# Performance work log

Measured on AMD Instinct MI355X. Metric: run time of the kernel, lower is better.

The kernel has to match this reference:

```python
import jax, jax.numpy as jnp
import numpy as np

B, T, D, H = 2, 2048, 1024, 16
DK = D // H
NEG = -1e9  # stand-in for -inf; causal mask guarantees >=1 valid key per row


def setup_inputs() -> dict:
    key = jax.random.key(0)
    ks = jax.random.split(key, 9)
    s = 1.0 / np.sqrt(D)
    x = jax.random.normal(ks[0], (B, T, D), dtype=jnp.float32)
    mask = jnp.broadcast_to(jnp.tril(jnp.ones((T, T), dtype=jnp.int32))[None, None], (B, 1, T, T))
    params = {}
    for i, n in enumerate(['q', 'k', 'v', 'o']):
        params['W' + n] = jax.random.normal(ks[1 + 2 * i], (D, D), dtype=jnp.float32) * s
        params['b' + n] = jax.random.normal(ks[2 + 2 * i], (D,), dtype=jnp.float32) * s
    return dict(x=x, mask=mask, **params)


def reference(x, mask, Wq, bq, Wk, bk, Wv, bv, Wo, bo):
    Bx, Tx, Dx = x.shape
    # projections: [B,T,D] -> [B,H,T,DK]
    def split_heads(y):
        return y.reshape(Bx, Tx, H, DK).transpose(0, 2, 1, 3)
    Q = split_heads(x @ Wq + bq)
    K = split_heads(x @ Wk + bk)
    V = split_heads(x @ Wv + bv)
    scores = jnp.einsum('bhqd,bhkd->bhqk', Q, K) / jnp.sqrt(jnp.float32(DK))
    scores = jnp.where(mask == 0, NEG, scores)
    attn = jax.nn.softmax(scores, axis=-1)  # dropout is identity in eval / p=0
    out = jnp.einsum('bhqk,bhkd->bhqd', attn, V)
    out = out.transpose(0, 2, 1, 3).reshape(Bx, Tx, Dx)
    return out @ Wo + bo
```

## Files before the change

kernel.cpp:

```cpp
#include <hip/hip_runtime.h>
#include <hip/hip_bf16.h>

typedef __bf16 bf16;
typedef __attribute__((ext_vector_type(8))) __bf16 bf16x8;
typedef __attribute__((ext_vector_type(4))) __bf16 bf16x4;
typedef __attribute__((ext_vector_type(4))) float f32x4;

#define TSEQ 2048
#define DMODEL 1024
#define NHEAD 16
#define DKH 64
#define BATCH 2
#define NQKV 3072

typedef __attribute__((address_space(1))) const void gv_t;
typedef __attribute__((address_space(3))) void sv_t;
__device__ __forceinline__ void gll16(const bf16* g, bf16* s) {
    __builtin_amdgcn_global_load_lds((gv_t*)g, (sv_t*)s, 16, 0, 0);
}
__device__ __forceinline__ void wait_vm0() {
    __builtin_amdgcn_s_waitcnt(0x0F70);
}

#define PREP_CONV 4096
#define PREP_TW   4096
#define PREP_GRID (PREP_CONV + PREP_TW + 12)
__global__ __launch_bounds__(256) void prep(
    const float* __restrict__ x,
    const float* __restrict__ Wq, const float* __restrict__ Wk,
    const float* __restrict__ Wv, const float* __restrict__ Wo,
    const float* __restrict__ bq, const float* __restrict__ bk,
    const float* __restrict__ bv,
    bf16* __restrict__ xb, bf16* __restrict__ WT, float* __restrict__ biasO)
{
    __shared__ float t[32][33];
    int bid = blockIdx.x;
    const int tid = threadIdx.x;
    if (bid < PREP_CONV) {
        int i = (bid * 256 + tid) * 4;
        f32x4 v = *(const f32x4*)(x + i);
        bf16x4 o;
#pragma unroll
        for (int j = 0; j < 4; ++j) o[j] = (bf16)v[j];
        *(bf16x4*)(xb + i) = o;
        return;
    }
    bid -= PREP_CONV;
    if (bid < PREP_TW) {
        int z = bid >> 10;
        int by = ((bid >> 5) & 31) * 32, bx = (bid & 31) * 32;
        const float* W = z == 0 ? Wq : z == 1 ? Wk : z == 2 ? Wv : Wo;
        bf16* T = WT + (size_t)z * DMODEL * DMODEL;
        int tx = tid & 31, ty = tid >> 5;
#pragma unroll
        for (int i = 0; i < 4; ++i)
            t[ty + i * 8][tx] = W[(size_t)(by + ty + i * 8) * DMODEL + bx + tx];
        __syncthreads();
#pragma unroll
        for (int i = 0; i < 4; ++i)
            T[(size_t)(bx + ty + i * 8) * DMODEL + by + tx] = (bf16)t[tx][ty + i * 8];
        return;
    }
    bid -= PREP_TW;
    int i = bid * 256 + tid;
    float v = i < 1024 ? bq[i] : i < 2048 ? bk[i - 1024] : bv[i - 2048];
    biasO[i] = v;
}

__global__ __launch_bounds__(256) void transpose_v(
    const bf16* __restrict__ QKV, bf16* __restrict__ VT)
{
    __shared__ bf16 t[32][33];
    int b = blockIdx.z >> 4, h = blockIdx.z & 15;
    int t0 = blockIdx.x * 32, d0 = blockIdx.y * 32;
    int tx = threadIdx.x, ty = threadIdx.y;
#pragma unroll
    for (int i = 0; i < 4; ++i)
        t[ty + i * 8][tx] =
            QKV[(size_t)(b * TSEQ + t0 + ty + i * 8) * NQKV + 2048 + h * DKH + d0 + tx];
    __syncthreads();
#pragma unroll
    for (int i = 0; i < 4; ++i)
        VT[((size_t)(b * NHEAD + h) * DKH + d0 + ty + i * 8) * TSEQ + t0 + tx] =
            t[tx][ty + i * 8];
}

template <typename OutT, int NW_N>
__global__ __launch_bounds__(256) void gemm_bias_kernel(
    const bf16* __restrict__ A, const bf16* __restrict__ BT,
    const float* __restrict__ bias, OutT* __restrict__ C, int ldc)
{
    constexpr int BN    = NW_N * 64;
    constexpr int MW    = 4 / NW_N;
    constexpr int WROWS = 128 / MW;
    constexpr int FM    = WROWS / 16;
    constexpr int ASZ   = 128 * 32;
    constexpr int BSZ   = BN * 32;
    constexpr int BNP   = BN + 4;
    constexpr int EPI   = sizeof(OutT) == 2 ? 128 * BN : 64 * BNP * 2;
    constexpr int SMEM  = (2 * ASZ + 2 * BSZ) > EPI ? (2 * ASZ + 2 * BSZ) : EPI;
    __shared__ bf16 smem[SMEM];
    bf16* As0 = smem;
    bf16* Bs0 = smem + 2 * ASZ;

    const int tid = threadIdx.x;
    const int ln = tid & 63, wave = tid >> 6;
    const int wm = NW_N == 2 ? (wave >> 1) : wave;
    const int wn = NW_N == 2 ? (wave & 1) : 0;
    const int lr = ln & 15, quad = ln >> 4;
    const int m0 = blockIdx.y * 128, n0 = blockIdx.x * BN;

    f32x4 acc[FM][4] = {};

    const int grow = ln >> 2;
    const int gcol = (ln & 3) * 8;
    const bf16* Ag = A + (size_t)(m0 + wave * 32 + grow) * DMODEL + gcol;
    const bf16* Bg = BT + (size_t)(n0 + (NW_N == 2 ? wave * 32 : wave * 16) + grow) * DMODEL + gcol;

    auto stage = [&](int buf, int kk) {
        bf16* AsW = As0 + buf * ASZ + wave * 1024;
        gll16(Ag + kk, AsW);
        gll16(Ag + (size_t)16 * DMODEL + kk, AsW + 512);
        if constexpr (NW_N == 2) {
            bf16* BsW = Bs0 + buf * BSZ + wave * 1024;
            gll16(Bg + kk, BsW);
            gll16(Bg + (size_t)16 * DMODEL + kk, BsW + 512);
        } else {
            gll16(Bg + kk, Bs0 + buf * BSZ + wave * 512);
        }
    };

    constexpr int NT = DMODEL / 32;
    stage(0, 0);
    wait_vm0();
    __syncthreads();
    for (int kt = 0; kt < NT; ++kt) {
        if (kt + 1 < NT) stage((kt + 1) & 1, (kt + 1) * 32);
        const bf16* AsB = As0 + (kt & 1) * ASZ;
        const bf16* BsB = Bs0 + (kt & 1) * BSZ;
        bf16x8 af[FM], bfr[4];
#pragma unroll
        for (int i = 0; i < FM; ++i)
            af[i] = *(const bf16x8*)(AsB + (wm * WROWS + i * 16 + lr) * 32 + quad * 8);
#pragma unroll
        for (int j = 0; j < 4; ++j)
            bfr[j] = *(const bf16x8*)(BsB + (wn * 64 + j * 16 + lr) * 32 + quad * 8);
#pragma unroll
        for (int i = 0; i < FM; ++i)
#pragma unroll
            for (int j = 0; j < 4; ++j)
                acc[i][j] = __builtin_amdgcn_mfma_f32_16x16x32_bf16(
                    af[i], bfr[j], acc[i][j], 0, 0, 0);
        wait_vm0();
        __syncthreads();
    }

    if constexpr (sizeof(OutT) == 2) {
        bf16* Cs = smem;
#pragma unroll
        for (int j = 0; j < 4; ++j) {
            int nl = wn * 64 + j * 16 + lr;
            float bv = bias[n0 + nl];
#pragma unroll
            for (int i = 0; i < FM; ++i) {
                int ml = wm * WROWS + i * 16 + quad * 4;
#pragma unroll
                for (int r = 0; r < 4; ++r)
                    Cs[(ml + r) * BN + nl] = (bf16)(acc[i][j][r] + bv);
            }
        }
        __syncthreads();
        constexpr int LPR = BN / 8;
        constexpr int RPP = 256 / LPR;
        const int rr = tid / LPR, cc = (tid % LPR) * 8;
#pragma unroll
        for (int p = 0; p < 128 / RPP; ++p) {
            int row = p * RPP + rr;
            *(bf16x8*)(C + (size_t)(m0 + row) * ldc + n0 + cc) =
                *(const bf16x8*)(Cs + row * BN + cc);
        }
    } else {
        float* Cf = (float*)smem;
#pragma unroll
        for (int half = 0; half < 2; ++half) {
            if (((wm * WROWS) >> 6) == half) {
#pragma unroll
                for (int j = 0; j < 4; ++j) {
                    int nl = wn * 64 + j * 16 + lr;
                    float bv = bias[n0 + nl];
#pragma unroll
                    for (int i = 0; i < FM; ++i) {
                        int ml = wm * WROWS + i * 16 + quad * 4 - half * 64;
#pragma unroll
                        for (int r = 0; r < 4; ++r)
                            Cf[(ml + r) * BNP + nl] = acc[i][j][r] + bv;
                    }
                }
            }
            __syncthreads();
            constexpr int LPR = BN / 4;
            constexpr int RPP = 256 / LPR;
            const int rr = tid / LPR, cc = (tid % LPR) * 4;
#pragma unroll
            for (int p = 0; p < 64 / RPP; ++p) {
                int row = p * RPP + rr;
                *(f32x4*)(C + (size_t)(m0 + half * 64 + row) * ldc + n0 + cc) =
                    *(const f32x4*)(Cf + row * BNP + cc);
            }
            __syncthreads();
        }
    }
}

template <bool MASK>
__device__ __forceinline__ void attn_chunk(
    int kc, int q0w, int lr, int quad,
    const bf16* __restrict__ KsB, const bf16* __restrict__ VsB,
    bf16* __restrict__ Pw,
    const bf16x8 qb[2], f32x4 oacc[4], float& lrow)
{
    const int sw = lr & 7;
    bf16x8 kb[4][2];
#pragma unroll
    for (int kt = 0; kt < 4; ++kt)
#pragma unroll
        for (int kk = 0; kk < 2; ++kk)
            kb[kt][kk] = *(const bf16x8*)(KsB + (kt * 16 + lr) * 64 +
                                          (((kk * 4 + quad) ^ sw) * 8));
    f32x4 st[4] = {};
#pragma unroll
    for (int kt = 0; kt < 4; ++kt)
#pragma unroll
        for (int kk = 0; kk < 2; ++kk)
            st[kt] = __builtin_amdgcn_mfma_f32_16x16x32_bf16(
                kb[kt][kk], qb[kk], st[kt], 0, 0, 0);

    const float scale2 = 0.18033688f;
    const int q = q0w + lr;
    float rs = 0.f;
#pragma unroll
    for (int kt = 0; kt < 4; ++kt) {
        bf16x4 p4;
#pragma unroll
        for (int r = 0; r < 4; ++r) {
            float p = exp2f(fmaf(st[kt][r], scale2, -24.0f));
            if (MASK && (kc + kt * 16 + quad * 4 + r > q)) p = 0.f;
            rs += p;
            p4[r] = (bf16)p;
        }
        *(bf16x4*)(Pw + lr * 64 + (((kt * 2 + (quad >> 1)) ^ sw) * 8) +
                   (quad & 1) * 4) = p4;
    }
    rs += __shfl_xor(rs, 16);
    rs += __shfl_xor(rs, 32);
    lrow += rs;

#pragma unroll
    for (int kk = 0; kk < 2; ++kk) {
        bf16x8 pa = *(const bf16x8*)(Pw + lr * 64 + (((kk * 4 + quad) ^ sw) * 8));
#pragma unroll
        for (int dt = 0; dt < 4; ++dt) {
            bf16x8 vb = *(const bf16x8*)(VsB + (dt * 16 + lr) * 64 +
                                         (((kk * 4 + quad) ^ sw) * 8));
            oacc[dt] = __builtin_amdgcn_mfma_f32_16x16x32_bf16(
                pa, vb, oacc[dt], 0, 0, 0);
        }
    }
}

__global__ __launch_bounds__(256, 4) void flash_attn(
    const bf16* __restrict__ QKV, const bf16* __restrict__ VT,
    bf16* __restrict__ O)
{
    __shared__ bf16 Ks[2][64 * 64];
    __shared__ bf16 Vs[2][64 * 64];
    __shared__ bf16 Pl[4][16 * 64];
    const int tid = threadIdx.x;
    const int ln = tid & 63, w = tid >> 6;
    const int lr = ln & 15, quad = ln >> 4;
    const int h = blockIdx.y, b = blockIdx.z;

    int xb = blockIdx.x;
    if ((h ^ b) & 1) xb = (TSEQ / 64 - 1) - xb;
    const int q0 = xb * 64;
    const int q0w = q0 + w * 16;
    bf16* Pw = Pl[w];

    const bf16* Qb = QKV + (size_t)b * TSEQ * NQKV + h * DKH;
    const bf16* Kb = Qb + 1024;
    const bf16* VTb = VT + (size_t)(b * NHEAD + h) * DKH * TSEQ;

    const int srow = (w & 1) * 32 + (ln >> 3);
    const int scol = ((ln & 7) ^ ((ln >> 3) & 7)) * 8;
    const bool stK = (w < 2);

    auto stage = [&](int buf, int kc) {
        if (stK) {
            const bf16* g = Kb + (size_t)(kc + srow) * NQKV + scol;
            bf16* s = &Ks[buf][(w & 1) * 32 * 64];
#pragma unroll
            for (int l = 0; l < 4; ++l)
                gll16(g + (size_t)(l * 8) * NQKV, s + l * 8 * 64);
        } else {
            const bf16* g = VTb + (size_t)srow * TSEQ + kc + scol;
            bf16* s = &Vs[buf][(w & 1) * 32 * 64];
#pragma unroll
            for (int l = 0; l < 4; ++l)
                gll16(g + (size_t)(l * 8) * TSEQ, s + l * 8 * 64);
        }
    };

    bf16x8 qb[2];
#pragma unroll
    for (int kk = 0; kk < 2; ++kk)
        qb[kk] = *(const bf16x8*)(Qb + (size_t)(q0w + lr) * NQKV +
                                  kk * 32 + quad * 8);

    f32x4 oacc[4] = {};
    float lrow = 0.f;

    const int nch = xb + 1;
    stage(0, 0);
    wait_vm0();
    __syncthreads();
    for (int c = 0; c < nch; ++c) {
        if (c + 1 < nch) stage((c + 1) & 1, (c + 1) * 64);
        const int kc = c * 64;
        if (c + 1 < nch)
            attn_chunk<false>(kc, q0w, lr, quad, Ks[c & 1], Vs[c & 1], Pw,
                              qb, oacc, lrow);
        else
            attn_chunk<true>(kc, q0w, lr, quad, Ks[c & 1], Vs[c & 1], Pw,
                             qb, oacc, lrow);
        wait_vm0();
        __syncthreads();
    }

#pragma unroll
    for (int r = 0; r < 4; ++r) {
        float inv = 1.0f / __shfl(lrow, quad * 4 + r);
        int row = q0w + quad * 4 + r;
#pragma unroll
        for (int dt = 0; dt < 4; ++dt)
            O[(size_t)(b * TSEQ + row) * DMODEL + h * DKH + dt * 16 + lr] =
                (bf16)(oacc[dt][r] * inv);
    }
}

extern "C" void kernel_launch(void* const* d_in, const int* in_sizes, int n_in,
                              void* d_out, int out_size, void* d_ws, size_t ws_size,
                              hipStream_t stream)
{
    const float* x  = (const float*)d_in[0];
    const float* Wq = (const float*)d_in[2];
    const float* bq = (const float*)d_in[3];
    const float* Wk = (const float*)d_in[4];
    const float* bk = (const float*)d_in[5];
    const float* Wv = (const float*)d_in[6];
    const float* bv = (const float*)d_in[7];
    const float* Wo = (const float*)d_in[8];
    const float* bo = (const float*)d_in[9];

    char* ws = (char*)d_ws;
    bf16* xb   = (bf16*)(ws);
    bf16* QKV  = (bf16*)(ws + (8u  << 20));
    bf16* VT   = (bf16*)(ws + (32u << 20));
    bf16* O    = (bf16*)(ws + (40u << 20));
    bf16* WT   = (bf16*)(ws + (48u << 20));
    float* wsBias = (float*)VT;

    prep<<<PREP_GRID, 256, 0, stream>>>(x, Wq, Wk, Wv, Wo, bq, bk, bv,
                                        xb, WT, wsBias);

    gemm_bias_kernel<bf16, 2><<<dim3(NQKV / 128, 32), 256, 0, stream>>>(
        xb, WT, wsBias, QKV, NQKV);

    dim3 tb(32, 8);
    transpose_v<<<dim3(TSEQ / 32, DKH / 32, BATCH * NHEAD), tb, 0, stream>>>(QKV, VT);

    flash_attn<<<dim3(TSEQ / 64, NHEAD, BATCH), 256, 0, stream>>>(QKV, VT, O);

    gemm_bias_kernel<float, 1><<<dim3(DMODEL / 64, 32), 256, 0, stream>>>(
        O, WT + 3u * (1u << 20), bo, (float*)d_out, DMODEL);
}
```

Before: 212.5 us.

## Triple-buffer GEMM and attention LDS staging with partial vmcnt waits

The GEMM and flash-attention loops move from double to triple-buffered global_load_lds staging, prefetching two tiles ahead. Each iteration waits only on the older tile's loads via a partial vmcnt and needs one barrier instead of a full drain. The attention kernel also raises wave priority around its MFMA blocks and lowers its launch-bounds occupancy hint from 4 to 2 to fit the larger LDS footprint. The extra buffers cost LDS and may reduce resident blocks per CU. Correctness depends on the per-thread load counts matching the vmcnt immediates.

```diff
diff --git a/kernel.cpp b/kernel.cpp
--- a/kernel.cpp
+++ b/kernel.cpp
@@ -18,9 +18,7 @@
 __device__ __forceinline__ void gll16(const bf16* g, bf16* s) {
     __builtin_amdgcn_global_load_lds((gv_t*)g, (sv_t*)s, 16, 0, 0);
 }
-__device__ __forceinline__ void wait_vm0() {
-    __builtin_amdgcn_s_waitcnt(0x0F70);
-}
+#define WAIT_VM(n) __builtin_amdgcn_s_waitcnt(0x0F70 | (n))
 
 #define PREP_CONV 4096
 #define PREP_TW   4096
@@ -98,10 +96,11 @@
     constexpr int BSZ   = BN * 32;
     constexpr int BNP   = BN + 4;
     constexpr int EPI   = sizeof(OutT) == 2 ? 128 * BN : 64 * BNP * 2;
-    constexpr int SMEM  = (2 * ASZ + 2 * BSZ) > EPI ? (2 * ASZ + 2 * BSZ) : EPI;
+    constexpr int STG   = 3 * ASZ + 3 * BSZ;
+    constexpr int SMEM  = STG > EPI ? STG : EPI;
     __shared__ bf16 smem[SMEM];
     bf16* As0 = smem;
-    bf16* Bs0 = smem + 2 * ASZ;
+    bf16* Bs0 = smem + 3 * ASZ;
 
     const int tid = threadIdx.x;
     const int ln = tid & 63, wave = tid >> 6;
@@ -132,12 +131,14 @@
 
     constexpr int NT = DMODEL / 32;
     stage(0, 0);
-    wait_vm0();
-    __syncthreads();
-    for (int kt = 0; kt < NT; ++kt) {
-        if (kt + 1 < NT) stage((kt + 1) & 1, (kt + 1) * 32);
-        const bf16* AsB = As0 + (kt & 1) * ASZ;
-        const bf16* BsB = Bs0 + (kt & 1) * BSZ;
+    stage(1, 32);
+    for (int kt = 0, cur = 0; kt < NT; ++kt, cur = cur == 2 ? 0 : cur + 1) {
+        if (kt + 1 < NT) { if constexpr (NW_N == 2) WAIT_VM(4); else WAIT_VM(3); }
+        else WAIT_VM(0);
+        __syncthreads();
+        if (kt + 2 < NT) stage(cur == 0 ? 2 : cur - 1, (kt + 2) * 32);
+        const bf16* AsB = As0 + cur * ASZ;
+        const bf16* BsB = Bs0 + cur * BSZ;
         bf16x8 af[FM], bfr[4];
 #pragma unroll
         for (int i = 0; i < FM; ++i)
@@ -151,9 +152,8 @@
             for (int j = 0; j < 4; ++j)
                 acc[i][j] = __builtin_amdgcn_mfma_f32_16x16x32_bf16(
                     af[i], bfr[j], acc[i][j], 0, 0, 0);
-        wait_vm0();
-        __syncthreads();
-    }
+    }
+    __syncthreads();
 
     if constexpr (sizeof(OutT) == 2) {
         bf16* Cs = smem;
@@ -228,12 +228,14 @@
             kb[kt][kk] = *(const bf16x8*)(KsB + (kt * 16 + lr) * 64 +
                                           (((kk * 4 + quad) ^ sw) * 8));
     f32x4 st[4] = {};
+    __builtin_amdgcn_s_setprio(1);
 #pragma unroll
     for (int kt = 0; kt < 4; ++kt)
 #pragma unroll
         for (int kk = 0; kk < 2; ++kk)
             st[kt] = __builtin_amdgcn_mfma_f32_16x16x32_bf16(
                 kb[kt][kk], qb[kk], st[kt], 0, 0, 0);
+    __builtin_amdgcn_s_setprio(0);
 
     const float scale2 = 0.18033688f;
     const int q = q0w + lr;
@@ -255,6 +257,7 @@
     rs += __shfl_xor(rs, 32);
     lrow += rs;
 
+    __builtin_amdgcn_s_setprio(1);
 #pragma unroll
     for (int kk = 0; kk < 2; ++kk) {
         bf16x8 pa = *(const bf16x8*)(Pw + lr * 64 + (((kk * 4 + quad) ^ sw) * 8));
@@ -266,14 +269,15 @@
                 pa, vb, oacc[dt], 0, 0, 0);
         }
     }
-}
-
-__global__ __launch_bounds__(256, 4) void flash_attn(
+    __builtin_amdgcn_s_setprio(0);
+}
+
+__global__ __launch_bounds__(256, 2) void flash_attn(
     const bf16* __restrict__ QKV, const bf16* __restrict__ VT,
     bf16* __restrict__ O)
 {
-    __shared__ bf16 Ks[2][64 * 64];
-    __shared__ bf16 Vs[2][64 * 64];
+    __shared__ bf16 Ks[3][64 * 64];
+    __shared__ bf16 Vs[3][64 * 64];
     __shared__ bf16 Pl[4][16 * 64];
     const int tid = threadIdx.x;
     const int ln = tid & 63, w = tid >> 6;
@@ -315,25 +319,25 @@
     for (int kk = 0; kk < 2; ++kk)
         qb[kk] = *(const bf16x8*)(Qb + (size_t)(q0w + lr) * NQKV +
                                   kk * 32 + quad * 8);
+    WAIT_VM(0);
 
     f32x4 oacc[4] = {};
     float lrow = 0.f;
 
     const int nch = xb + 1;
     stage(0, 0);
-    wait_vm0();
-    __syncthreads();
-    for (int c = 0; c < nch; ++c) {
-        if (c + 1 < nch) stage((c + 1) & 1, (c + 1) * 64);
+    if (nch > 1) stage(1, 64);
+    for (int c = 0, cur = 0; c < nch; ++c, cur = cur == 2 ? 0 : cur + 1) {
+        if (c + 1 < nch) WAIT_VM(4); else WAIT_VM(0);
+        __syncthreads();
+        if (c + 2 < nch) stage(cur == 0 ? 2 : cur - 1, (c + 2) * 64);
         const int kc = c * 64;
         if (c + 1 < nch)
-            attn_chunk<false>(kc, q0w, lr, quad, Ks[c & 1], Vs[c & 1], Pw,
+            attn_chunk<false>(kc, q0w, lr, quad, Ks[cur], Vs[cur], Pw,
                               qb, oacc, lrow);
         else
-            attn_chunk<true>(kc, q0w, lr, quad, Ks[c & 1], Vs[c & 1], Pw,
+            attn_chunk<true>(kc, q0w, lr, quad, Ks[cur], Vs[cur], Pw,
                              qb, oacc, lrow);
-        wait_vm0();
-        __syncthreads();
     }
 
 #pragma unroll
```

New measurement: 240.0 us. +12.9%, slower.

## Fuse V transpose into QKV GEMM epilogue and pair query tiles in attention

Applied to the files above, without the earlier changes.

The QKV GEMM epilogue now writes V tiles directly in transposed layout through shared memory, so the separate transpose_v kernel and its launch and global round trip go away. The flash attention kernel processes two query tiles per workgroup, one short and one long (p and 31-p). This balances causal work across workgroups and shares each K/V stage between both tiles. In exchange it doubles accumulator registers, lowers the occupancy hint to 2, and adds more mode branches.

```diff
diff --git a/kernel.cpp b/kernel.cpp
--- a/kernel.cpp
+++ b/kernel.cpp
@@ -18,9 +18,7 @@
 __device__ __forceinline__ void gll16(const bf16* g, bf16* s) {
     __builtin_amdgcn_global_load_lds((gv_t*)g, (sv_t*)s, 16, 0, 0);
 }
-__device__ __forceinline__ void wait_vm0() {
-    __builtin_amdgcn_s_waitcnt(0x0F70);
-}
+#define WAIT_VM(n) __builtin_amdgcn_s_waitcnt(0x0F70 | (n))
 
 #define PREP_CONV 4096
 #define PREP_TW   4096
@@ -67,28 +65,11 @@
     biasO[i] = v;
 }
 
-__global__ __launch_bounds__(256) void transpose_v(
-    const bf16* __restrict__ QKV, bf16* __restrict__ VT)
-{
-    __shared__ bf16 t[32][33];
-    int b = blockIdx.z >> 4, h = blockIdx.z & 15;
-    int t0 = blockIdx.x * 32, d0 = blockIdx.y * 32;
-    int tx = threadIdx.x, ty = threadIdx.y;
-#pragma unroll
-    for (int i = 0; i < 4; ++i)
-        t[ty + i * 8][tx] =
-            QKV[(size_t)(b * TSEQ + t0 + ty + i * 8) * NQKV + 2048 + h * DKH + d0 + tx];
-    __syncthreads();
-#pragma unroll
-    for (int i = 0; i < 4; ++i)
-        VT[((size_t)(b * NHEAD + h) * DKH + d0 + ty + i * 8) * TSEQ + t0 + tx] =
-            t[tx][ty + i * 8];
-}
-
-template <typename OutT, int NW_N>
+template <typename OutT, int NW_N, bool FUSE_VT>
 __global__ __launch_bounds__(256) void gemm_bias_kernel(
     const bf16* __restrict__ A, const bf16* __restrict__ BT,
-    const float* __restrict__ bias, OutT* __restrict__ C, int ldc)
+    const float* __restrict__ bias, OutT* __restrict__ C, int ldc,
+    bf16* __restrict__ VT)
 {
     constexpr int BN    = NW_N * 64;
     constexpr int MW    = 4 / NW_N;
@@ -97,8 +78,11 @@
     constexpr int ASZ   = 128 * 32;
     constexpr int BSZ   = BN * 32;
     constexpr int BNP   = BN + 4;
-    constexpr int EPI   = sizeof(OutT) == 2 ? 128 * BN : 64 * BNP * 2;
-    constexpr int SMEM  = (2 * ASZ + 2 * BSZ) > EPI ? (2 * ASZ + 2 * BSZ) : EPI;
+    constexpr int TST   = 136;
+    constexpr int EPI   = sizeof(OutT) == 2 ? (FUSE_VT ? 128 * TST : 128 * BN)
+                                            : 64 * BNP * 2;
+    constexpr int STG   = 2 * ASZ + 2 * BSZ;
+    constexpr int SMEM  = STG > EPI ? STG : EPI;
     __shared__ bf16 smem[SMEM];
     bf16* As0 = smem;
     bf16* Bs0 = smem + 2 * ASZ;
@@ -132,7 +116,7 @@
 
     constexpr int NT = DMODEL / 32;
     stage(0, 0);
-    wait_vm0();
+    WAIT_VM(0);
     __syncthreads();
     for (int kt = 0; kt < NT; ++kt) {
         if (kt + 1 < NT) stage((kt + 1) & 1, (kt + 1) * 32);
@@ -151,11 +135,38 @@
             for (int j = 0; j < 4; ++j)
                 acc[i][j] = __builtin_amdgcn_mfma_f32_16x16x32_bf16(
                     af[i], bfr[j], acc[i][j], 0, 0, 0);
-        wait_vm0();
+        WAIT_VM(0);
         __syncthreads();
     }
 
     if constexpr (sizeof(OutT) == 2) {
+        if (FUSE_VT && n0 >= 2048) {
+            bf16* Cs = smem;
+#pragma unroll
+            for (int j = 0; j < 4; ++j) {
+                int nl = wn * 64 + j * 16 + lr;
+                float bv = bias[n0 + nl];
+#pragma unroll
+                for (int i = 0; i < FM; ++i) {
+                    int ml = wm * WROWS + i * 16 + quad * 4;
+#pragma unroll
+                    for (int r = 0; r < 4; ++r)
+                        Cs[nl * TST + ml + r] = (bf16)(acc[i][j][r] + bv);
+                }
+            }
+            __syncthreads();
+            const int bb = m0 >> 11;
+            const int tloc = m0 & 2047;
+#pragma unroll
+            for (int p = 0; p < 8; ++p) {
+                int dl = p * 16 + (tid >> 4);
+                int t0 = (tid & 15) * 8;
+                bf16x8 v = *(const bf16x8*)(Cs + dl * TST + t0);
+                *(bf16x8*)(VT + (size_t)(bb * 1024 + (n0 - 2048) + dl) * TSEQ +
+                           tloc + t0) = v;
+            }
+            return;
+        }
         bf16* Cs = smem;
 #pragma unroll
         for (int j = 0; j < 4; ++j) {
@@ -213,12 +224,39 @@
 }
 
 template <bool MASK>
+__device__ __forceinline__ float softmax_store(
+    const f32x4 st[4], bf16* __restrict__ Pw,
+    int qrow, int kc, int lr, int quad, int sw)
+{
+    const float scale2 = 0.18033688f;
+    float rs = 0.f;
+#pragma unroll
+    for (int kt = 0; kt < 4; ++kt) {
+        bf16x4 p4;
+#pragma unroll
+        for (int r = 0; r < 4; ++r) {
+            float p = exp2f(fmaf(st[kt][r], scale2, -24.0f));
+            if (MASK && (kc + kt * 16 + quad * 4 + r > qrow)) p = 0.f;
+            rs += p;
+            p4[r] = (bf16)p;
+        }
+        *(bf16x4*)(Pw + lr * 64 + (((kt * 2 + (quad >> 1)) ^ sw) * 8) +
+                   (quad & 1) * 4) = p4;
+    }
+    rs += __shfl_xor(rs, 16);
+    rs += __shfl_xor(rs, 32);
+    return rs;
+}
+
+template <int MODE>
 __device__ __forceinline__ void attn_chunk(
-    int kc, int q0w, int lr, int quad,
+    int kc, int qA, int qB, int lr, int quad,
     const bf16* __restrict__ KsB, const bf16* __restrict__ VsB,
-    bf16* __restrict__ Pw,
-    const bf16x8 qb[2], f32x4 oacc[4], float& lrow)
-{
+    bf16* __restrict__ PwA, bf16* __restrict__ PwB,
+    const bf16x8 qbA[2], const bf16x8 qbB[2],
+    f32x4 oA[4], f32x4 oB[4], float& lA, float& lB)
+{
+    constexpr bool TWO = (MODE < 2);
     const int sw = lr & 7;
     bf16x8 kb[4][2];
 #pragma unroll
@@ -227,64 +265,64 @@
         for (int kk = 0; kk < 2; ++kk)
             kb[kt][kk] = *(const bf16x8*)(KsB + (kt * 16 + lr) * 64 +
                                           (((kk * 4 + quad) ^ sw) * 8));
-    f32x4 st[4] = {};
+    f32x4 stB[4] = {};
 #pragma unroll
     for (int kt = 0; kt < 4; ++kt)
 #pragma unroll
         for (int kk = 0; kk < 2; ++kk)
-            st[kt] = __builtin_amdgcn_mfma_f32_16x16x32_bf16(
-                kb[kt][kk], qb[kk], st[kt], 0, 0, 0);
-
-    const float scale2 = 0.18033688f;
-    const int q = q0w + lr;
-    float rs = 0.f;
-#pragma unroll
-    for (int kt = 0; kt < 4; ++kt) {
-        bf16x4 p4;
-#pragma unroll
-        for (int r = 0; r < 4; ++r) {
-            float p = exp2f(fmaf(st[kt][r], scale2, -24.0f));
-            if (MASK && (kc + kt * 16 + quad * 4 + r > q)) p = 0.f;
-            rs += p;
-            p4[r] = (bf16)p;
-        }
-        *(bf16x4*)(Pw + lr * 64 + (((kt * 2 + (quad >> 1)) ^ sw) * 8) +
-                   (quad & 1) * 4) = p4;
-    }
-    rs += __shfl_xor(rs, 16);
-    rs += __shfl_xor(rs, 32);
-    lrow += rs;
+            stB[kt] = __builtin_amdgcn_mfma_f32_16x16x32_bf16(
+                kb[kt][kk], qbB[kk], stB[kt], 0, 0, 0);
+    f32x4 stA[4] = {};
+    if constexpr (TWO) {
+#pragma unroll
+        for (int kt = 0; kt < 4; ++kt)
+#pragma unroll
+            for (int kk = 0; kk < 2; ++kk)
+                stA[kt] = __builtin_amdgcn_mfma_f32_16x16x32_bf16(
+                    kb[kt][kk], qbA[kk], stA[kt], 0, 0, 0);
+    }
+
+    lB += softmax_store<MODE == 3>(stB, PwB, qB, kc, lr, quad, sw);
+    if constexpr (TWO)
+        lA += softmax_store<MODE == 1>(stA, PwA, qA, kc, lr, quad, sw);
 
 #pragma unroll
     for (int kk = 0; kk < 2; ++kk) {
-        bf16x8 pa = *(const bf16x8*)(Pw + lr * 64 + (((kk * 4 + quad) ^ sw) * 8));
+        bf16x8 pb = *(const bf16x8*)(PwB + lr * 64 + (((kk * 4 + quad) ^ sw) * 8));
+        bf16x8 pa;
+        if constexpr (TWO)
+            pa = *(const bf16x8*)(PwA + lr * 64 + (((kk * 4 + quad) ^ sw) * 8));
 #pragma unroll
         for (int dt = 0; dt < 4; ++dt) {
             bf16x8 vb = *(const bf16x8*)(VsB + (dt * 16 + lr) * 64 +
                                          (((kk * 4 + quad) ^ sw) * 8));
-            oacc[dt] = __builtin_amdgcn_mfma_f32_16x16x32_bf16(
-                pa, vb, oacc[dt], 0, 0, 0);
-        }
-    }
-}
-
-__global__ __launch_bounds__(256, 4) void flash_attn(
+            oB[dt] = __builtin_amdgcn_mfma_f32_16x16x32_bf16(
+                pb, vb, oB[dt], 0, 0, 0);
+            if constexpr (TWO)
+                oA[dt] = __builtin_amdgcn_mfma_f32_16x16x32_bf16(
+                    pa, vb, oA[dt], 0, 0, 0);
+        }
+    }
+}
+
+__global__ __launch_bounds__(256, 2) void flash_attn(
     const bf16* __restrict__ QKV, const bf16* __restrict__ VT,
     bf16* __restrict__ O)
 {
     __shared__ bf16 Ks[2][64 * 64];
     __shared__ bf16 Vs[2][64 * 64];
-    __shared__ bf16 Pl[4][16 * 64];
+    __shared__ bf16 Pl[8][16 * 64];
     const int tid = threadIdx.x;
     const int ln = tid & 63, w = tid >> 6;
     const int lr = ln & 15, quad = ln >> 4;
-    const int h = blockIdx.y, b = blockIdx.z;
-
-    int xb = blockIdx.x;
-    if ((h ^ b) & 1) xb = (TSEQ / 64 - 1) - xb;
-    const int q0 = xb * 64;
-    const int q0w = q0 + w * 16;
-    bf16* Pw = Pl[w];
+    const int wg = blockIdx.x;
+    const int g = wg & 31, p = wg >> 5;
+    const int h = g >> 1, b = g & 1;
+    const int xbA = p, xbB = 31 - p;
+    const int q0A = xbA * 64, q0B = xbB * 64;
+    const int qA = q0A + w * 16 + lr, qB = q0B + w * 16 + lr;
+    bf16* PwA = Pl[w];
+    bf16* PwB = Pl[4 + w];
 
     const bf16* Qb = QKV + (size_t)b * TSEQ * NQKV + h * DKH;
     const bf16* Kb = Qb + 1024;
@@ -296,54 +334,69 @@
 
     auto stage = [&](int buf, int kc) {
         if (stK) {
-            const bf16* g = Kb + (size_t)(kc + srow) * NQKV + scol;
+            const bf16* g2 = Kb + (size_t)(kc + srow) * NQKV + scol;
             bf16* s = &Ks[buf][(w & 1) * 32 * 64];
 #pragma unroll
             for (int l = 0; l < 4; ++l)
-                gll16(g + (size_t)(l * 8) * NQKV, s + l * 8 * 64);
+                gll16(g2 + (size_t)(l * 8) * NQKV, s + l * 8 * 64);
         } else {
-            const bf16* g = VTb + (size_t)srow * TSEQ + kc + scol;
+            const bf16* g2 = VTb + (size_t)srow * TSEQ + kc + scol;
             bf16* s = &Vs[buf][(w & 1) * 32 * 64];
 #pragma unroll
             for (int l = 0; l < 4; ++l)
-                gll16(g + (size_t)(l * 8) * TSEQ, s + l * 8 * 64);
+                gll16(g2 + (size_t)(l * 8) * TSEQ, s + l * 8 * 64);
         }
     };
 
-    bf16x8 qb[2];
-#pragma unroll
-    for (int kk = 0; kk < 2; ++kk)
-        qb[kk] = *(const bf16x8*)(Qb + (size_t)(q0w + lr) * NQKV +
-                                  kk * 32 + quad * 8);
-
-    f32x4 oacc[4] = {};
-    float lrow = 0.f;
-
-    const int nch = xb + 1;
+    bf16x8 qbA[2], qbB[2];
+#pragma unroll
+    for (int kk = 0; kk < 2; ++kk) {
+        qbA[kk] = *(const bf16x8*)(Qb + (size_t)qA * NQKV + kk * 32 + quad * 8);
+        qbB[kk] = *(const bf16x8*)(Qb + (size_t)qB * NQKV + kk * 32 + quad * 8);
+    }
+    WAIT_VM(0);
+
+    f32x4 oA[4] = {}, oB[4] = {};
+    float lA = 0.f, lB = 0.f;
+
+    const int nld = xbB + 1;
     stage(0, 0);
-    wait_vm0();
+    WAIT_VM(0);
     __syncthreads();
-    for (int c = 0; c < nch; ++c) {
-        if (c + 1 < nch) stage((c + 1) & 1, (c + 1) * 64);
+    for (int c = 0; c < nld; ++c) {
+        if (c + 1 < nld) stage((c + 1) & 1, (c + 1) * 64);
         const int kc = c * 64;
-        if (c + 1 < nch)
-            attn_chunk<false>(kc, q0w, lr, quad, Ks[c & 1], Vs[c & 1], Pw,
-                              qb, oacc, lrow);
+        const bf16* K = Ks[c & 1];
+        const bf16* V = Vs[c & 1];
+        if (c < xbA)
+            attn_chunk<0>(kc, qA, qB, lr, quad, K, V, PwA, PwB, qbA, qbB, oA, oB, lA, lB);
+        else if (c == xbA)
+            attn_chunk<1>(kc, qA, qB, lr, quad, K, V, PwA, PwB, qbA, qbB, oA, oB, lA, lB);
+        else if (c == nld - 1)
+            attn_chunk<3>(kc, qA, qB, lr, quad, K, V, PwA, PwB, qbA, qbB, oA, oB, lA, lB);
         else
-            attn_chunk<true>(kc, q0w, lr, quad, Ks[c & 1], Vs[c & 1], Pw,
-                             qb, oacc, lrow);
-        wait_vm0();
+            attn_chunk<2>(kc, qA, qB, lr, quad, K, V, PwA, PwB, qbA, qbB, oA, oB, lA, lB);
+        WAIT_VM(0);
         __syncthreads();
     }
 
 #pragma unroll
     for (int r = 0; r < 4; ++r) {
-        float inv = 1.0f / __shfl(lrow, quad * 4 + r);
-        int row = q0w + quad * 4 + r;
+        float invB = 1.0f / __shfl(lB, quad * 4 + r);
+        int rowB = q0B + w * 16 + quad * 4 + r;
 #pragma unroll
         for (int dt = 0; dt < 4; ++dt)
-            O[(size_t)(b * TSEQ + row) * DMODEL + h * DKH + dt * 16 + lr] =
-                (bf16)(oacc[dt][r] * inv);
+            O[(size_t)(b * TSEQ + rowB) * DMODEL + h * DKH + dt * 16 + lr] =
+                (bf16)(oB[dt][r] * invB);
+    }
+#pragma unroll
+    for (int r = 0; r < 4; ++r) {
+        float invA = 1.0f / __shfl(lA, quad * 4 + r);
+        int rowA = q0A + w * 16 + quad * 4 + r;
+#pragma unroll
+        for (int dt = 0; dt < 4; ++dt)
+            O[(size_t)(b * TSEQ + rowA) * DMODEL + h * DKH + dt * 16 + lr] =
+                (bf16)(oA[dt][r] * invA);
     }
 }
 
@@ -367,19 +420,16 @@
     bf16* VT   = (bf16*)(ws + (32u << 20));
     bf16* O    = (bf16*)(ws + (40u << 20));
     bf16* WT   = (bf16*)(ws + (48u << 20));
-    float* wsBias = (float*)VT;
+    float* wsBias = (float*)O;
 
     prep<<<PREP_GRID, 256, 0, stream>>>(x, Wq, Wk, Wv, Wo, bq, bk, bv,
                                         xb, WT, wsBias);
 
-    gemm_bias_kernel<bf16, 2><<<dim3(NQKV / 128, 32), 256, 0, stream>>>(
-        xb, WT, wsBias, QKV, NQKV);
-
-    dim3 tb(32, 8);
-    transpose_v<<<dim3(TSEQ / 32, DKH / 32, BATCH * NHEAD), tb, 0, stream>>>(QKV, VT);
-
-    flash_attn<<<dim3(TSEQ / 64, NHEAD, BATCH), 256, 0, stream>>>(QKV, VT, O);
-
-    gemm_bias_kernel<float, 1><<<dim3(DMODEL / 64, 32), 256, 0, stream>>>(
-        O, WT + 3u * (1u << 20), bo, (float*)d_out, DMODEL);
-}
+    gemm_bias_kernel<bf16, 2, true><<<dim3(NQKV / 128, 32), 256, 0, stream>>>(
+        xb, WT, wsBias, QKV, NQKV, VT);
+
+    flash_attn<<<512, 256, 0, stream>>>(QKV, VT, O);
+
+    gemm_bias_kernel<float, 1, false><<<dim3(DMODEL / 64, 32), 256, 0, stream>>>(
+        O, WT + 3u * (1u << 20), bo, (float*)d_out, DMODEL, nullptr);
+}
```

Result: no change. 208.4 us (-1.9%).
